# Optimization experiments

Hardware: AMD Instinct MI355X
Metric: run time of the kernel (lower is better)

## Reference

```python
import jax, jax.numpy as jnp
import numpy as np

D_MODEL = 768; D_STATE = 64; D_CONV = 4; EXPAND = 2
D_INNER = EXPAND * D_MODEL            # 1536
HEADDIM = 64; NHEADS = D_INNER // HEADDIM  # 24
NGROUPS = 1
CONV_DIM = D_INNER + 2 * NGROUPS * D_STATE        # 1664
D_IN_PROJ = 2 * D_INNER + 2 * NGROUPS * D_STATE + NHEADS  # 3224
B_SZ = 2; SEQ = 4096
EPS = 1e-5


def setup_inputs() -> dict:
    key = jax.random.key(0)
    ks = jax.random.split(key, 10)
    s = 0.02
    return {
        "x": jax.random.normal(ks[0], (B_SZ, SEQ, D_MODEL), jnp.float32),
        "ln_w": jnp.ones((D_MODEL,), jnp.float32),
        "ln_b": jnp.zeros((D_MODEL,), jnp.float32),
        "in_proj_w": jax.random.normal(ks[1], (D_MODEL, D_IN_PROJ), jnp.float32) * s,
        "conv_w": jax.random.normal(ks[2], (CONV_DIM, D_CONV), jnp.float32) * s,
        "conv_b": jnp.zeros((CONV_DIM,), jnp.float32),
        "dt_bias": jax.random.uniform(ks[3], (NHEADS,), jnp.float32, -4.6, -2.0),
        "A_log": jnp.log(jnp.arange(1, NHEADS + 1, dtype=jnp.float32)),
        "D_param": jnp.ones((NHEADS,), jnp.float32),
        "rms_w": jnp.ones((D_INNER,), jnp.float32),
        "out_proj_w": jax.random.normal(ks[4], (D_INNER, D_MODEL), jnp.float32) * s,
        "gate_w": jax.random.normal(ks[5], (D_MODEL, D_MODEL), jnp.float32) * s,
        "gate_b": jnp.zeros((D_MODEL,), jnp.float32),
        "out_w": jax.random.normal(ks[6], (D_MODEL, D_MODEL), jnp.float32) * s,
        "out_b": jnp.zeros((D_MODEL,), jnp.float32),
    }


def _silu(u):
    return u * jax.nn.sigmoid(u)


def _causal_conv1d(x, w, b):
    # x: [B,L,C], w: [C,K] depthwise, left-padded causal conv
    K = w.shape[1]
    L = x.shape[1]
    xp = jnp.pad(x, ((0, 0), (K - 1, 0), (0, 0)))
    y = b
    for k in range(K):
        y = y + xp[:, k:k + L, :] * w[:, k]
    return y


def _selective_scan(xh, dt, A, Bm, Cm):
    # xh: [B,L,H,P], dt: [B,L,H], A: [H], Bm/Cm: [B,L,N] (ngroups=1)
    dA = jnp.exp(dt * A)  # [B,L,H]
    # time-major for scan
    dA_t = jnp.moveaxis(dA, 1, 0)            # [L,B,H]
    dt_t = jnp.moveaxis(dt, 1, 0)            # [L,B,H]
    x_t = jnp.moveaxis(xh, 1, 0)             # [L,B,H,P]
    B_t = jnp.moveaxis(Bm, 1, 0)             # [L,B,N]
    C_t = jnp.moveaxis(Cm, 1, 0)             # [L,B,N]

    h0 = jnp.zeros((xh.shape[0], NHEADS, HEADDIM, D_STATE), xh.dtype)

    def step(h, inp):
        da, dtv, xv, bv, cv = inp
        # dBx: [B,H,P,N] built per-step to avoid materializing [B,L,H,P,N]
        dBx = (dtv[:, :, None] * xv)[..., None] * bv[:, None, None, :]
        h = h * da[:, :, None, None] + dBx
        y = jnp.einsum('bhpn,bn->bhp', h, cv)
        return h, y

    _, ys = jax.lax.scan(step, h0, (dA_t, dt_t, x_t, B_t, C_t))
    return jnp.moveaxis(ys, 0, 1)  # [B,L,H,P]


def _mamba2(xn, in_proj_w, conv_w, conv_b, dt_bias, A_log, D_param, rms_w, out_proj_w):
    zxbcdt = xn @ in_proj_w  # [B,L,D_IN_PROJ]
    z = zxbcdt[..., :D_INNER]
    xBC = zxbcdt[..., D_INNER:D_INNER + CONV_DIM]
    dt = zxbcdt[..., D_INNER + CONV_DIM:]

    xBC = _silu(_causal_conv1d(xBC, conv_w, conv_b))
    xh = xBC[..., :D_INNER]
    Bm = xBC[..., D_INNER:D_INNER + NGROUPS * D_STATE]
    Cm = xBC[..., D_INNER + NGROUPS * D_STATE:]

    dt = jax.nn.softplus(dt + dt_bias)        # [B,L,H]
    A = -jnp.exp(A_log)                       # [H]

    B, L = xh.shape[0], xh.shape[1]
    xh = xh.reshape(B, L, NHEADS, HEADDIM)
    y = _selective_scan(xh, dt, A, Bm, Cm)
    y = y + xh * D_param[None, None, :, None]  # skip connection D*x
    y = y.reshape(B, L, D_INNER)

    # gated RMSNorm: rmsnorm(y * silu(z)) * w
    y = y * _silu(z)
    y = y * jax.lax.rsqrt(jnp.mean(y * y, axis=-1, keepdims=True) + EPS) * rms_w
    return y @ out_proj_w


def reference(x, ln_w, ln_b, in_proj_w, conv_w, conv_b, dt_bias, A_log, D_param,
              rms_w, out_proj_w, gate_w, gate_b, out_w, out_b):
    mu = jnp.mean(x, axis=-1, keepdims=True)
    var = jnp.mean((x - mu) ** 2, axis=-1, keepdims=True)
    x_norm = (x - mu) * jax.lax.rsqrt(var + EPS) * ln_w + ln_b

    y = _mamba2(x_norm, in_proj_w, conv_w, conv_b, dt_bias, A_log, D_param, rms_w, out_proj_w)
    gate = jax.nn.sigmoid(x_norm @ gate_w + gate_b)
    y_gated = y * gate
    return x + y_gated @ out_w + out_b
```

## Files before the change

kernel.cpp:

```cpp
#include <hip/hip_runtime.h>
#include <hip/hip_bf16.h>
#include <cstddef>

#define DMODEL  768
#define DINNER  1536
#define DSTATE  64
#define NH      24
#define HD      64
#define CONVD   1664
#define DINPROJ 3224
#define SEQ     4096
#define BSZ     2
#define NTOK    8192
#define NCHUNK  64
#define EPSF    1e-5f
#define LP      72

typedef __attribute__((ext_vector_type(8))) short  short8;
typedef __attribute__((ext_vector_type(4))) float  f32x4;

__device__ __forceinline__ unsigned short f2bf(float f) {
  union { float f; unsigned int u; } v; v.f = f;
  unsigned int r = v.u + 0x7fffu + ((v.u >> 16) & 1u);
  return (unsigned short)(r >> 16);
}
__device__ __forceinline__ float bf2f(unsigned short u) {
  union { unsigned int i; float f; } v; v.i = ((unsigned int)u) << 16; return v.f;
}
__device__ __forceinline__ unsigned long long pack4bf(float a, float b, float c, float d) {
  return (unsigned long long)(f2bf(a) | ((unsigned int)f2bf(b) << 16))
       | ((unsigned long long)(f2bf(c) | ((unsigned int)f2bf(d) << 16)) << 32);
}
__device__ __forceinline__ float sigm(float x) { return 1.f / (1.f + __expf(-x)); }

__device__ __forceinline__ void gld16(const unsigned short* g, unsigned short* l) {
  __builtin_amdgcn_global_load_lds(
      (const __attribute__((address_space(1))) unsigned int*)g,
      (__attribute__((address_space(3))) unsigned int*)l, 16, 0, 0);
}

__device__ __forceinline__ void xcd_tiles(int& m0, int& n0) {
  const int nt = gridDim.x, mt = gridDim.y;
  const int id = blockIdx.y * nt + blockIdx.x;
  const int mper = mt >> 3;
  const int xcd = id & 7, within = id >> 3;
  m0 = (xcd * mper + (within % mper)) * 128;
  n0 = (within / mper) * 128;
}

__global__ __launch_bounds__(256) void k_ln(const float* __restrict__ x,
    const float* __restrict__ w, const float* __restrict__ b,
    unsigned short* __restrict__ xn)
{
  __shared__ float red[4];
  const int row = blockIdx.x, tid = threadIdx.x;
  const float* xr = x + (size_t)row * DMODEL;
  float v[3]; float s = 0.f;
  #pragma unroll
  for (int q = 0; q < 3; q++) { v[q] = xr[q*256 + tid]; s += v[q]; }
  #pragma unroll
  for (int off = 32; off; off >>= 1) s += __shfl_down(s, off);
  if ((tid & 63) == 0) red[tid >> 6] = s;
  __syncthreads();
  const float mu = (red[0] + red[1] + red[2] + red[3]) * (1.f / DMODEL);
  __syncthreads();
  float s2 = 0.f;
  #pragma unroll
  for (int q = 0; q < 3; q++) { float d = v[q] - mu; s2 += d * d; }
  #pragma unroll
  for (int off = 32; off; off >>= 1) s2 += __shfl_down(s2, off);
  if ((tid & 63) == 0) red[tid >> 6] = s2;
  __syncthreads();
  const float rs = rsqrtf((red[0] + red[1] + red[2] + red[3]) * (1.f / DMODEL) + EPSF);
  unsigned short* xo = xn + (size_t)row * DMODEL;
  #pragma unroll
  for (int q = 0; q < 3; q++) {
    int col = q*256 + tid;
    xo[col] = f2bf((v[q] - mu) * rs * w[col] + b[col]);
  }
}

__global__ __launch_bounds__(256) void k_wtrans4(
    const float* __restrict__ W0, unsigned short* __restrict__ T0,
    const float* __restrict__ W1, unsigned short* __restrict__ T1,
    const float* __restrict__ W2, unsigned short* __restrict__ T2,
    const float* __restrict__ W3, unsigned short* __restrict__ T3)
{
  const float* W; unsigned short* T; int K, N;
  switch (blockIdx.z) {
    case 0:  W = W0; T = T0; K = 768;  N = 3224; break;
    case 1:  W = W1; T = T1; K = 768;  N = 768;  break;
    case 2:  W = W2; T = T2; K = 1536; N = 768;  break;
    default: W = W3; T = T3; K = 768;  N = 768;  break;
  }
  const int n0 = blockIdx.x * 32, k0 = blockIdx.y * 32;
  if (n0 >= N || k0 >= K) return;
  __shared__ float tile[32][33];
  const int tid = threadIdx.x;
  const int tx = tid & 31, ty = tid >> 5;
  #pragma unroll
  for (int r = 0; r < 4; r++) {
    int k = k0 + ty + 8*r;
    if (k < K && n0 + tx < N) tile[ty + 8*r][tx] = W[(size_t)k * N + n0 + tx];
  }
  __syncthreads();
  #pragma unroll
  for (int r = 0; r < 4; r++) {
    int n = n0 + ty + 8*r, k = k0 + tx;
    if (n < N && k < K) T[(size_t)n * K + k] = f2bf(tile[tx][ty + 8*r]);
  }
}

__device__ __forceinline__ void gemm_core(const unsigned short* __restrict__ A,
    const unsigned short* __restrict__ Bt, float* __restrict__ C,
    unsigned short* __restrict__ Cb,
    int M, int N, int K, int epi, const float* __restrict__ bias,
    const float* __restrict__ resid, int m0, int n0,
    unsigned short* As, unsigned short* Bs)
{
  const int tid = threadIdx.x;
  const int lane = tid & 63, w = tid >> 6;
  const int wm = (w >> 1) * 64, wn = (w & 1) * 64;
  const int l15 = lane & 15, lq = lane >> 4;
  const int sw = l15 & 7;
  f32x4 acc[4][4];
  #pragma unroll
  for (int i = 0; i < 4; i++)
    #pragma unroll
    for (int j = 0; j < 4; j++) acc[i][j] = (f32x4){0.f, 0.f, 0.f, 0.f};

  int rowg[4], gq[4];
  #pragma unroll
  for (int r = 0; r < 4; r++) {
    int gi = (r * 4 + w) * 64 + lane;
    rowg[r] = gi >> 3;
    gq[r] = (gi & 7) ^ (rowg[r] & 7);
  }

  for (int k0 = 0; k0 < K; k0 += 64) {
    __syncthreads();
    #pragma unroll
    for (int r = 0; r < 4; r++)
      gld16(A + (size_t)(m0 + rowg[r]) * K + k0 + gq[r] * 8, &As[(r * 4 + w) * 512]);
    #pragma unroll
    for (int r = 0; r < 4; r++) {
      int nr = n0 + rowg[r]; if (nr >= N) nr = N - 1;
      gld16(Bt + (size_t)nr * K + k0 + gq[r] * 8, &Bs[(r * 4 + w) * 512]);
    }
    __syncthreads();
    #pragma unroll
    for (int ks = 0; ks < 2; ks++) {
      short8 a8[4], b8[4];
      #pragma unroll
      for (int mi = 0; mi < 4; mi++)
        a8[mi] = *(const short8*)(&As[(wm + 16 * mi + l15) * 64 + ((lq + 4 * ks) ^ sw) * 8]);
      #pragma unroll
      for (int ni = 0; ni < 4; ni++)
        b8[ni] = *(const short8*)(&Bs[(wn + 16 * ni + l15) * 64 + ((lq + 4 * ks) ^ sw) * 8]);
      #pragma unroll
      for (int mi = 0; mi < 4; mi++)
        #pragma unroll
        for (int ni = 0; ni < 4; ni++)
          acc[mi][ni] = __builtin_amdgcn_mfma_f32_16x16x32_bf16(a8[mi], b8[ni], acc[mi][ni], 0, 0, 0);
    }
  }
  #pragma unroll
  for (int mi = 0; mi < 4; mi++) {
    #pragma unroll
    for (int r = 0; r < 4; r++) {
      int row = m0 + wm + 16*mi + lq*4 + r;
      #pragma unroll
      for (int ni = 0; ni < 4; ni++) {
        int col = n0 + wn + 16*ni + l15;
        if (col < N) {
          float vv = acc[mi][ni][r];
          if (epi == 1)      vv = sigm(vv + bias[col]);
          else if (epi == 2) vv = vv + bias[col] + resid[(size_t)row * N + col];
          if (Cb) Cb[(size_t)row * N + col] = f2bf(vv);
          else    C [(size_t)row * N + col] = vv;
        }
      }
    }
  }
}

__global__ __launch_bounds__(256) void k_gemm(const unsigned short* __restrict__ A,
    const unsigned short* __restrict__ Bt, float* __restrict__ C,
    unsigned short* __restrict__ Cb,
    int M, int N, int K, int epi, const float* __restrict__ bias,
    const float* __restrict__ resid)
{
  __shared__ alignas(16) unsigned short As[128 * 64];
  __shared__ alignas(16) unsigned short Bs[128 * 64];
  int m0, n0;
  xcd_tiles(m0, n0);
  gemm_core(A, Bt, C, Cb, M, N, K, epi, bias, resid, m0, n0, As, Bs);
}

__global__ __launch_bounds__(256) void k_dualgemm(
    const unsigned short* __restrict__ A0, const unsigned short* __restrict__ B0,
    unsigned short* __restrict__ C0, int K0,
    const unsigned short* __restrict__ A1, const unsigned short* __restrict__ B1,
    unsigned short* __restrict__ C1, int K1, const float* __restrict__ bias1, int N)
{
  __shared__ alignas(16) unsigned short As[128 * 64];
  __shared__ alignas(16) unsigned short Bs[128 * 64];
  int m0, n0;
  xcd_tiles(m0, n0);
  if (blockIdx.z == 0)
    gemm_core(A0, B0, nullptr, C0, NTOK, N, K0, 0, nullptr, nullptr, m0, n0, As, Bs);
  else
    gemm_core(A1, B1, nullptr, C1, NTOK, N, K1, 1, bias1, nullptr, m0, n0, As, Bs);
}

__global__ __launch_bounds__(256) void k_conv(const unsigned short* __restrict__ zx,
    const float* __restrict__ cw, const float* __restrict__ cb,
    unsigned short* __restrict__ out)
{
  __shared__ alignas(8) unsigned short tile[67][132];
  const int tid = threadIdx.x;
  const int c0 = blockIdx.x * 128;
  const int tc = blockIdx.y;
  const int t0 = tc * 64;
  const bool haloOK = (tc & 63) != 0;
  for (int i = tid; i < 67 * 16; i += 256) {
    int row = i >> 4, g = i & 15;
    unsigned long long v0 = 0, v1 = 0;
    if (row >= 3 || haloOK) {
      const unsigned short* p = zx + (size_t)(t0 - 3 + row) * DINPROJ + DINNER + c0 + g * 8;
      v0 = *(const unsigned long long*)p;
      v1 = *(const unsigned long long*)(p + 4);
    }
    *(unsigned long long*)(&tile[row][g * 8])     = v0;
    *(unsigned long long*)(&tile[row][g * 8 + 4]) = v1;
  }
  __syncthreads();
  const int ch0 = (tid & 63) * 2;
  const int trow = tid >> 6;
  const int cg = c0 + ch0;
  float cw0[4], cw1[4];
  #pragma unroll
  for (int k = 0; k < 4; k++) { cw0[k] = cw[cg * 4 + k]; cw1[k] = cw[(cg + 1) * 4 + k]; }
  const float cb0 = cb[cg], cb1 = cb[cg + 1];
  #pragma unroll
  for (int q = 0; q < 16; q++) {
    int tq = trow * 16 + q;
    float a0 = cb0, a1 = cb1;
    #pragma unroll
    for (int k = 0; k < 4; k++) {
      unsigned int u = *(const unsigned int*)(&tile[tq + k][ch0]);
      a0 += bf2f((unsigned short)u) * cw0[k];
      a1 += bf2f((unsigned short)(u >> 16)) * cw1[k];
    }
    float s0 = a0 * sigm(a0), s1 = a1 * sigm(a1);
    *(unsigned int*)(out + (size_t)(t0 + tq) * CONVD + cg) =
        (unsigned int)f2bf(s0) | ((unsigned int)f2bf(s1) << 16);
  }
}

__global__ __launch_bounds__(256) void k_chunkstate(const unsigned short* __restrict__ zx,
    const unsigned short* __restrict__ xbcc, const float* __restrict__ dt_bias,
    const float* __restrict__ A_log, float* __restrict__ S, float* __restrict__ CD)
{
  const int c = blockIdx.x, bh = blockIdx.y;
  const int b = bh / NH, h = bh % NH;
  const int tid = threadIdx.x;
  const int lane = tid & 63, w = tid >> 6;
  const int l15 = lane & 15, lq = lane >> 4;
  __shared__ float wv_[64];
  __shared__ alignas(16) unsigned short Bwt[64][LP];
  __shared__ alignas(16) unsigned short Xt [64][LP];

  if (tid < 64) {
    int t = c * 64 + tid;
    float xx = bf2f(zx[((size_t)(b * SEQ + t)) * DINPROJ + (DINNER + CONVD) + h]) + dt_bias[h];
    float dt_ = (xx > 15.f) ? xx : log1pf(__expf(xx));
    float Ah = -__expf(A_log[h]);
    float v = dt_ * Ah;
    #pragma unroll
    for (int off = 1; off < 64; off <<= 1) {
      float u = __shfl_up(v, off);
      if (tid >= off) v += u;
    }
    float L63 = __shfl(v, 63);
    wv_[tid] = __expf(L63 - v) * dt_;
    if (tid == 63) CD[bh * 64 + c] = __expf(v);
  }
  unsigned long long braw[4];
  #pragma unroll
  for (int it = 0; it < 4; it++) {
    int i4 = tid + 256 * it;
    int s = i4 >> 4, q4 = (i4 & 15) * 4;
    size_t rb = ((size_t)(b * SEQ) + c * 64 + s) * CONVD;
    braw[it] = *(const unsigned long long*)(xbcc + rb + DINNER + q4);
    unsigned short xs[4];
    *(unsigned long long*)xs = *(const unsigned long long*)(xbcc + rb + h * HD + q4);
    Xt[q4+0][s] = xs[0]; Xt[q4+1][s] = xs[1]; Xt[q4+2][s] = xs[2]; Xt[q4+3][s] = xs[3];
  }
  __syncthreads();
  #pragma unroll
  for (int it = 0; it < 4; it++) {
    int i4 = tid + 256 * it;
    int s = i4 >> 4, q4 = (i4 & 15) * 4;
    float wsc = wv_[s];
    unsigned short us[4];
    *(unsigned long long*)us = braw[it];
    Bwt[q4+0][s] = f2bf(bf2f(us[0]) * wsc);
    Bwt[q4+1][s] = f2bf(bf2f(us[1]) * wsc);
    Bwt[q4+2][s] = f2bf(bf2f(us[2]) * wsc);
    Bwt[q4+3][s] = f2bf(bf2f(us[3]) * wsc);
  }
  __syncthreads();
  const int n0 = 16 * w;
  short8 a0 = *(const short8*)(&Bwt[n0 + l15][lq * 8]);
  short8 a1 = *(const short8*)(&Bwt[n0 + l15][32 + lq * 8]);
  size_t sb = ((size_t)bh * 64 + c) * 4096;
  #pragma unroll
  for (int pt = 0; pt < 4; pt++) {
    f32x4 acc = (f32x4){0.f, 0.f, 0.f, 0.f};
    short8 b0 = *(const short8*)(&Xt[16*pt + l15][lq * 8]);
    short8 b1 = *(const short8*)(&Xt[16*pt + l15][32 + lq * 8]);
    acc = __builtin_amdgcn_mfma_f32_16x16x32_bf16(a0, b0, acc, 0, 0, 0);
    acc = __builtin_amdgcn_mfma_f32_16x16x32_bf16(a1, b1, acc, 0, 0, 0);
    #pragma unroll
    for (int r = 0; r < 4; r++) {
      int n = n0 + 4*lq + r, p = 16*pt + l15;
      S[sb + (size_t)n * 64 + p] = acc[r];
    }
  }
}

__global__ __launch_bounds__(256) void k_chunkrec(float* __restrict__ S,
    const float* __restrict__ CD)
{
  const int bh = blockIdx.x >> 4, part = blockIdx.x & 15;
  const int e = part * 256 + threadIdx.x;
  float g = 0.f;
  size_t base = (size_t)bh * 64 * 4096 + e;
  for (int c = 0; c < 64; c++) {
    size_t ad = base + (size_t)c * 4096;
    float sv = S[ad];
    float pc = CD[bh * 64 + c];
    S[ad] = g;
    g = pc * g + sv;
  }
}

__global__ __launch_bounds__(256) void k_chunkout(const unsigned short* __restrict__ zx,
    const unsigned short* __restrict__ xbcc, const float* __restrict__ S,
    const float* __restrict__ dt_bias, const float* __restrict__ A_log,
    const float* __restrict__ Dp, unsigned short* __restrict__ Y)
{
  const int c = blockIdx.x, bh = blockIdx.y;
  const int b = bh / NH, h = bh % NH;
  const int tid = threadIdx.x;
  const int lane = tid & 63, w = tid >> 6;
  const int l15 = lane & 15, lq = lane >> 4;
  __shared__ float dts[64], Lc[64], ein[64];
  __shared__ alignas(16) unsigned short Cs  [64][LP];
  __shared__ alignas(16) unsigned short BsPs[64][LP];
  __shared__ alignas(16) unsigned short Xt  [64][LP];
  __shared__ alignas(16) unsigned short Gt  [64][LP];

  if (tid < 64) {
    int t = c * 64 + tid;
    float xx = bf2f(zx[((size_t)(b * SEQ + t)) * DINPROJ + (DINNER + CONVD) + h]) + dt_bias[h];
    float dt_ = (xx > 15.f) ? xx : log1pf(__expf(xx));
    dts[tid] = dt_;
    float Ah = -__expf(A_log[h]);
    float v = dt_ * Ah;
    #pragma unroll
    for (int off = 1; off < 64; off <<= 1) {
      float u = __shfl_up(v, off);
      if (tid >= off) v += u;
    }
    Lc[tid] = v;
    ein[tid] = __expf(v);
  }
  const size_t gslot = ((size_t)bh * 64 + c) * 4096;
  #pragma unroll
  for (int it = 0; it < 4; it++) {
    int i4 = tid + 256 * it;
    int rr = i4 >> 4, q4 = (i4 & 15) * 4;
    size_t rb = ((size_t)(b * SEQ) + c * 64 + rr) * CONVD;
    const unsigned short* pC = xbcc + rb + (DINNER + DSTATE) + q4;
    Cs[rr][q4+0] = pC[0]; Cs[rr][q4+1] = pC[1]; Cs[rr][q4+2] = pC[2]; Cs[rr][q4+3] = pC[3];
    const unsigned short* pB = xbcc + rb + DINNER + q4;
    BsPs[rr][q4+0] = pB[0]; BsPs[rr][q4+1] = pB[1]; BsPs[rr][q4+2] = pB[2]; BsPs[rr][q4+3] = pB[3];
    unsigned short xs[4];
    *(unsigned long long*)xs = *(const unsigned long long*)(xbcc + rb + h * HD + q4);
    Xt[q4+0][rr] = xs[0]; Xt[q4+1][rr] = xs[1]; Xt[q4+2][rr] = xs[2]; Xt[q4+3][rr] = xs[3];
    float4 vG = *(const float4*)(S + gslot + (size_t)i4 * 4);
    Gt[q4+0][rr] = f2bf(vG.x); Gt[q4+1][rr] = f2bf(vG.y);
    Gt[q4+2][rr] = f2bf(vG.z); Gt[q4+3][rr] = f2bf(vG.w);
  }
  __syncthreads();
  const int i0 = 16 * w;
  short8 ac0 = *(const short8*)(&Cs[i0 + l15][lq * 8]);
  short8 ac1 = *(const short8*)(&Cs[i0 + l15][32 + lq * 8]);
  float pp[4][4];
  #pragma unroll
  for (int st = 0; st < 4; st++) {
    f32x4 g = (f32x4){0.f, 0.f, 0.f, 0.f};
    if (st <= w) {
      short8 b0 = *(const short8*)(&BsPs[16*st + l15][lq * 8]);
      short8 b1 = *(const short8*)(&BsPs[16*st + l15][32 + lq * 8]);
      g = __builtin_amdgcn_mfma_f32_16x16x32_bf16(ac0, b0, g, 0, 0, 0);
      g = __builtin_amdgcn_mfma_f32_16x16x32_bf16(ac1, b1, g, 0, 0, 0);
    }
    #pragma unroll
    for (int r = 0; r < 4; r++) {
      int i = i0 + 4*lq + r, s = 16*st + l15;
      pp[st][r] = (s <= i) ? g[r] * __expf(Lc[i] - Lc[s]) * dts[s] : 0.f;
    }
  }
  __syncthreads();
  #pragma unroll
  for (int st = 0; st < 4; st++)
    #pragma unroll
    for (int r = 0; r < 4; r++)
      BsPs[i0 + 4*lq + r][16*st + l15] = f2bf(pp[st][r]);
  __syncthreads();
  short8 ap0 = *(const short8*)(&BsPs[i0 + l15][lq * 8]);
  short8 ap1 = *(const short8*)(&BsPs[i0 + l15][32 + lq * 8]);
  const float Dh = Dp[h];
  #pragma unroll
  for (int pt = 0; pt < 4; pt++) {
    const int p0 = 16 * pt;
    f32x4 y1 = (f32x4){0.f, 0.f, 0.f, 0.f};
    f32x4 y2 = (f32x4){0.f, 0.f, 0.f, 0.f};
    short8 bx0 = *(const short8*)(&Xt[p0 + l15][lq * 8]);
    y1 = __builtin_amdgcn_mfma_f32_16x16x32_bf16(ap0, bx0, y1, 0, 0, 0);
    if (w >= 2) {
      short8 bx1 = *(const short8*)(&Xt[p0 + l15][32 + lq * 8]);
      y1 = __builtin_amdgcn_mfma_f32_16x16x32_bf16(ap1, bx1, y1, 0, 0, 0);
    }
    short8 bg0 = *(const short8*)(&Gt[p0 + l15][lq * 8]);
    short8 bg1 = *(const short8*)(&Gt[p0 + l15][32 + lq * 8]);
    y2 = __builtin_amdgcn_mfma_f32_16x16x32_bf16(ac0, bg0, y2, 0, 0, 0);
    y2 = __builtin_amdgcn_mfma_f32_16x16x32_bf16(ac1, bg1, y2, 0, 0, 0);
    #pragma unroll
    for (int r = 0; r < 4; r++) {
      int i = i0 + 4*lq + r, p = p0 + l15;
      float xv = bf2f(Xt[p][i]);
      float o = y1[r] + ein[i] * y2[r] + Dh * xv;
      Y[((size_t)(b * SEQ) + c * 64 + i) * DINNER + h * HD + p] = f2bf(o);
    }
  }
}

__global__ __launch_bounds__(256) void k_fuse(const unsigned short* __restrict__ Y,
    const unsigned short* __restrict__ ZX, const float* __restrict__ rw,
    unsigned short* __restrict__ YN)
{
  __shared__ float red[4];
  const int row = blockIdx.x, tid = threadIdx.x;
  const unsigned short* yr = Y + (size_t)row * DINNER;
  const unsigned short* zr = ZX + (size_t)row * DINPROJ;
  float v[6]; float s2 = 0.f;
  #pragma unroll
  for (int q = 0; q < 6; q++) {
    int col = q * 256 + tid;
    float z = bf2f(zr[col]);
    float yv = bf2f(yr[col]) * (z * sigm(z));
    v[q] = yv; s2 += yv * yv;
  }
  #pragma unroll
  for (int off = 32; off; off >>= 1) s2 += __shfl_down(s2, off);
  if ((tid & 63) == 0) red[tid >> 6] = s2;
  __syncthreads();
  const float rs = rsqrtf((red[0] + red[1] + red[2] + red[3]) * (1.f / DINNER) + EPSF);
  unsigned short* yo = YN + (size_t)row * DINNER;
  #pragma unroll
  for (int q = 0; q < 6; q++) {
    int col = q * 256 + tid;
    yo[col] = f2bf(v[q] * rs * rw[col]);
  }
}

__global__ __launch_bounds__(256) void k_gatemul(const unsigned short* __restrict__ YP,
    const unsigned short* __restrict__ G, unsigned short* __restrict__ YG)
{
  size_t i4 = ((size_t)blockIdx.x * 256 + threadIdx.x) * 4;
  unsigned short a[4], b[4];
  *(unsigned long long*)a = *(const unsigned long long*)(YP + i4);
  *(unsigned long long*)b = *(const unsigned long long*)(G + i4);
  *(unsigned long long*)(YG + i4) = pack4bf(
      bf2f(a[0]) * bf2f(b[0]), bf2f(a[1]) * bf2f(b[1]),
      bf2f(a[2]) * bf2f(b[2]), bf2f(a[3]) * bf2f(b[3]));
}

extern "C" void kernel_launch(void* const* d_in, const int* in_sizes, int n_in,
                              void* d_out, int out_size, void* d_ws, size_t ws_size,
                              hipStream_t stream)
{
  const float* x         = (const float*)d_in[0];
  const float* ln_w      = (const float*)d_in[1];
  const float* ln_b      = (const float*)d_in[2];
  const float* in_proj_w = (const float*)d_in[3];
  const float* conv_w    = (const float*)d_in[4];
  const float* conv_b    = (const float*)d_in[5];
  const float* dt_bias   = (const float*)d_in[6];
  const float* A_log     = (const float*)d_in[7];
  const float* D_param   = (const float*)d_in[8];
  const float* rms_w     = (const float*)d_in[9];
  const float* out_proj_w= (const float*)d_in[10];
  const float* gate_w    = (const float*)d_in[11];
  const float* gate_b    = (const float*)d_in[12];
  const float* out_w     = (const float*)d_in[13];
  const float* out_b     = (const float*)d_in[14];
  float* out = (float*)d_out;
  char* ws = (char*)d_ws;

  const size_t WS_NEEDED = 177848320ull;
  if (ws_size < WS_NEEDED) return;

  unsigned short* XN    = (unsigned short*)(ws + 0);
  unsigned short* WIT   = (unsigned short*)(ws + 12582912);
  unsigned short* WGT   = (unsigned short*)(ws + 17534976);
  unsigned short* WOPT  = (unsigned short*)(ws + 18714624);
  unsigned short* WOT   = (unsigned short*)(ws + 21073920);
  unsigned short* ZXb   = (unsigned short*)(ws + 22253568);
  unsigned short* XBCCb = (unsigned short*)(ws + 75075584);
  float*          SG    = (float*)(ws + 102338560);
  float*          CD    = (float*)(ws + 152670208);
  unsigned short* Yb    = (unsigned short*)(ws + 152682496);
  unsigned short* YN    = (unsigned short*)(ws + 102338560);
  unsigned short* Gb    = (unsigned short*)(ws + 22253568);
  unsigned short* YPb   = (unsigned short*)(ws + 34836480);
  unsigned short* YG    = (unsigned short*)(ws + 75075584);

  k_wtrans4<<<dim3(101, 48, 4), 256, 0, stream>>>(in_proj_w, WIT, gate_w, WGT,
                                                  out_proj_w, WOPT, out_w, WOT);
  k_ln<<<NTOK, 256, 0, stream>>>(x, ln_w, ln_b, XN);
  k_gemm<<<dim3(26, 64), 256, 0, stream>>>(XN, WIT, nullptr, ZXb, NTOK, DINPROJ, DMODEL, 0, nullptr, nullptr);
  k_conv<<<dim3(13, 128), 256, 0, stream>>>(ZXb, conv_w, conv_b, XBCCb);
  k_chunkstate<<<dim3(NCHUNK, BSZ * NH), 256, 0, stream>>>(ZXb, XBCCb, dt_bias, A_log, SG, CD);
  k_chunkrec<<<BSZ * NH * 16, 256, 0, stream>>>(SG, CD);
  k_chunkout<<<dim3(NCHUNK, BSZ * NH), 256, 0, stream>>>(ZXb, XBCCb, SG, dt_bias, A_log, D_param, Yb);
  k_fuse<<<NTOK, 256, 0, stream>>>(Yb, ZXb, rms_w, YN);
  k_dualgemm<<<dim3(6, 64, 2), 256, 0, stream>>>(YN, WOPT, YPb, DINNER,
                                                 XN, WGT, Gb, DMODEL, gate_b, DMODEL);
  k_gatemul<<<(NTOK * DMODEL / 4) / 256, 256, 0, stream>>>(YPb, Gb, YG);
  k_gemm<<<dim3(6, 64), 256, 0, stream>>>(YG, WOT, out, nullptr, NTOK, DMODEL, DMODEL, 2, out_b, x);
}
```

Before: 410.7 us.

## Double-buffer GEMM shared-memory tiles to overlap global loads with MFMA compute

Splits the A and B LDS tiles into two buffers. The next K-slice is prefetched into the idle buffer while MFMAs consume the current one, and one of the two barriers per K-step is removed. The aim is to hide global-load latency inside the shared GEMM core used by the single and dual GEMM kernels. In exchange, LDS use per block doubles to 64 KB, which may lower occupancy.

```diff
diff --git a/kernel.cpp b/kernel.cpp
--- a/kernel.cpp
+++ b/kernel.cpp
@@ -15,6 +15,7 @@
 #define NCHUNK  64
 #define EPSF    1e-5f
 #define LP      72
+#define BUFS    8192
 
 typedef __attribute__((ext_vector_type(8))) short  short8;
 typedef __attribute__((ext_vector_type(4))) float  f32x4;
@@ -129,40 +130,55 @@
     #pragma unroll
     for (int j = 0; j < 4; j++) acc[i][j] = (f32x4){0.f, 0.f, 0.f, 0.f};
 
-  int rowg[4], gq[4];
+  int rowg[4], gq[4], nrg[4];
   #pragma unroll
   for (int r = 0; r < 4; r++) {
     int gi = (r * 4 + w) * 64 + lane;
     rowg[r] = gi >> 3;
     gq[r] = (gi & 7) ^ (rowg[r] & 7);
-  }
-
+    int nr = n0 + rowg[r]; if (nr >= N) nr = N - 1;
+    nrg[r] = nr;
+  }
+
+  #pragma unroll
+  for (int r = 0; r < 4; r++)
+    gld16(A + (size_t)(m0 + rowg[r]) * K + gq[r] * 8, &As[(r * 4 + w) * 512]);
+  #pragma unroll
+  for (int r = 0; r < 4; r++)
+    gld16(Bt + (size_t)nrg[r] * K + gq[r] * 8, &Bs[(r * 4 + w) * 512]);
+
+  int p = 0;
   for (int k0 = 0; k0 < K; k0 += 64) {
     __syncthreads();
-    #pragma unroll
-    for (int r = 0; r < 4; r++)
-      gld16(A + (size_t)(m0 + rowg[r]) * K + k0 + gq[r] * 8, &As[(r * 4 + w) * 512]);
-    #pragma unroll
-    for (int r = 0; r < 4; r++) {
-      int nr = n0 + rowg[r]; if (nr >= N) nr = N - 1;
-      gld16(Bt + (size_t)nr * K + k0 + gq[r] * 8, &Bs[(r * 4 + w) * 512]);
-    }
-    __syncthreads();
+    if (k0 + 64 < K) {
+      const int pn = p ^ 1;
+      #pragma unroll
+      for (int r = 0; r < 4; r++)
+        gld16(A + (size_t)(m0 + rowg[r]) * K + (k0 + 64) + gq[r] * 8,
+              &As[pn * BUFS + (r * 4 + w) * 512]);
+      #pragma unroll
+      for (int r = 0; r < 4; r++)
+        gld16(Bt + (size_t)nrg[r] * K + (k0 + 64) + gq[r] * 8,
+              &Bs[pn * BUFS + (r * 4 + w) * 512]);
+    }
+    const unsigned short* Ab = As + p * BUFS;
+    const unsigned short* Bb = Bs + p * BUFS;
     #pragma unroll
     for (int ks = 0; ks < 2; ks++) {
       short8 a8[4], b8[4];
       #pragma unroll
       for (int mi = 0; mi < 4; mi++)
-        a8[mi] = *(const short8*)(&As[(wm + 16 * mi + l15) * 64 + ((lq + 4 * ks) ^ sw) * 8]);
+        a8[mi] = *(const short8*)(&Ab[(wm + 16 * mi + l15) * 64 + ((lq + 4 * ks) ^ sw) * 8]);
       #pragma unroll
       for (int ni = 0; ni < 4; ni++)
-        b8[ni] = *(const short8*)(&Bs[(wn + 16 * ni + l15) * 64 + ((lq + 4 * ks) ^ sw) * 8]);
+        b8[ni] = *(const short8*)(&Bb[(wn + 16 * ni + l15) * 64 + ((lq + 4 * ks) ^ sw) * 8]);
       #pragma unroll
       for (int mi = 0; mi < 4; mi++)
         #pragma unroll
         for (int ni = 0; ni < 4; ni++)
           acc[mi][ni] = __builtin_amdgcn_mfma_f32_16x16x32_bf16(a8[mi], b8[ni], acc[mi][ni], 0, 0, 0);
     }
+    p ^= 1;
   }
   #pragma unroll
   for (int mi = 0; mi < 4; mi++) {
@@ -190,8 +206,8 @@
     int M, int N, int K, int epi, const float* __restrict__ bias,
     const float* __restrict__ resid)
 {
-  __shared__ alignas(16) unsigned short As[128 * 64];
-  __shared__ alignas(16) unsigned short Bs[128 * 64];
+  __shared__ alignas(16) unsigned short As[2 * BUFS];
+  __shared__ alignas(16) unsigned short Bs[2 * BUFS];
   int m0, n0;
   xcd_tiles(m0, n0);
   gemm_core(A, Bt, C, Cb, M, N, K, epi, bias, resid, m0, n0, As, Bs);
@@ -203,8 +219,8 @@
     const unsigned short* __restrict__ A1, const unsigned short* __restrict__ B1,
     unsigned short* __restrict__ C1, int K1, const float* __restrict__ bias1, int N)
 {
-  __shared__ alignas(16) unsigned short As[128 * 64];
-  __shared__ alignas(16) unsigned short Bs[128 * 64];
+  __shared__ alignas(16) unsigned short As[2 * BUFS];
+  __shared__ alignas(16) unsigned short Bs[2 * BUFS];
   int m0, n0;
   xcd_tiles(m0, n0);
   if (blockIdx.z == 0)
```

Result: faster. 395.9 us (-3.6%).
